# Kernel optimization log

Measured on AMD Instinct MI355X. Metric: run time of the kernel, lower is better.

The kernel has to match this reference:

```python
import jax, jax.numpy as jnp
import numpy as np
from jax import lax

UP = 2
K = 3
IN_C, OUT_C = 64, 64
PAD = K // 2  # 1
WEIGHT_GAIN = 1.0 / np.sqrt(IN_C * K * K)
ACT_GAIN = np.sqrt(2.0)  # lrelu def_gain
CLAMP = 256.0
LRELU_ALPHA = 0.2


def setup_inputs() -> dict:
    key = jax.random.key(0)
    k1, k2 = jax.random.split(key)
    x = jax.random.normal(k1, (16, IN_C, 128, 128), dtype=jnp.float32)
    weight = jax.random.normal(k2, (OUT_C, IN_C, K, K), dtype=jnp.float32)
    bias = jnp.zeros((OUT_C,), dtype=jnp.float32)
    # upfirdn2d.setup_filter((1,3,3,1)): outer product, normalized to sum 1
    a = jnp.array([1.0, 3.0, 3.0, 1.0], dtype=jnp.float32)
    f = jnp.outer(a, a)
    f = f / jnp.sum(f)  # 4x4 separable FIR filter
    return {"x": x, "weight": weight, "bias": bias, "f": f}


def _upfirdn2d_up2(x, f):
    # zero-insertion upsample by 2 + pad + FIR filter, gain = up**2
    N, C, H, W = x.shape
    fw = f.shape[-1]  # 4
    # conv2d_resample padding adjustment for up>1 on top of base padding k//2
    p0 = PAD + (fw + UP - 1) // 2  # 3
    p1 = PAD + (fw - UP) // 2      # 2
    fk = jnp.tile((f * (UP * UP))[None, None], (C, 1, 1, 1))  # [C,1,4,4] depthwise
    # lhs_dilation=2 gives 2H-1 samples; add (UP-1) extra right/bottom zeros to
    # match upfirdn's 2H zero-inserted signal.
    return lax.conv_general_dilated(
        x, fk, window_strides=(1, 1),
        padding=((p0, p1 + UP - 1), (p0, p1 + UP - 1)),
        lhs_dilation=(UP, UP),
        feature_group_count=C,
        dimension_numbers=("NCHW", "OIHW", "NCHW"))


def reference(x, weight, bias, f):
    h = _upfirdn2d_up2(x, f)  # [N, C, 2H+2, 2W+2]
    # conv: flip_weight = (up == 1) = False -> true convolution (flip kernel)
    w = (weight * WEIGHT_GAIN)[:, :, ::-1, ::-1]
    y = lax.conv_general_dilated(
        h, w, window_strides=(1, 1), padding="VALID",
        dimension_numbers=("NCHW", "OIHW", "NCHW"))  # [N, OUT_C, 2H, 2W]
    # fused bias + lrelu + gain + clamp (bias_act with gain=1)
    y = y + bias[None, :, None, None]
    y = jnp.where(y >= 0, y, LRELU_ALPHA * y) * ACT_GAIN
    y = jnp.clip(y, -CLAMP, CLAMP)
    return y
```

## Files before the change

### kernel.cpp

```cpp
#include <hip/hip_runtime.h>

typedef float f32x16 __attribute__((ext_vector_type(16)));
typedef float f32x4  __attribute__((ext_vector_type(4)));
typedef float f32x2  __attribute__((ext_vector_type(2)));
typedef short bf16x8 __attribute__((ext_vector_type(8)));

#define NB 16
#define CI 64
#define CO 64
#define Hh 128
#define Ww 128

__device__ short g_A[9 * 4 * 8 * 64 * 8];
__device__ short g_xh[(size_t)NB * Hh * Ww * CI];

__device__ inline short f2bf(float f) {
  union { float f; unsigned u; } v; v.f = f;
  unsigned r = (v.u + 0x7FFF + ((v.u >> 16) & 1)) >> 16;
  return (short)r;
}

__global__ __launch_bounds__(256) void prep(const float* __restrict__ x,
                                            const float* __restrict__ w) {
  const int tid = threadIdx.x;
  if (blockIdx.x >= 2048) {
    const int base = (blockIdx.x - 2048) * 2304;
    #pragma unroll
    for (int i = 0; i < 9; ++i) {
      const int ef = base + i * 256 + tid;
      const int e   = ef & 7;
      const int l   = (ef >> 3) & 63;
      const int mg  = (ef >> 9) & 7;
      const int ks  = (ef >> 12) & 3;
      const int tap = ef >> 14;
      const int r   = l & 31;
      const int px  = r & 1;
      const int py  = mg >> 2;
      const int oc  = (mg & 3) * 16 + (r >> 1);
      const int ic  = ks * 16 + (l >> 5) * 8 + e;
      const int dyi = tap / 3, dxi = tap % 3;
      const int my = 2 * dyi + 1 - py;
      const int mx = 2 * dxi + 1 - px;
      const float FF[4] = {0.25f, 0.75f, 0.75f, 0.25f};
      const float* wp = w + (oc * CI + ic) * 9;
      float s = 0.f;
      #pragma unroll
      for (int ky = 0; ky < 3; ++ky) {
        const int iy = my - ky;
        if (iy < 0 || iy > 3) continue;
        #pragma unroll
        for (int kx = 0; kx < 3; ++kx) {
          const int ix = mx - kx;
          if (ix < 0 || ix > 3) continue;
          s += wp[(2 - ky) * 3 + (2 - kx)] * (FF[iy] * FF[ix]);
        }
      }
      g_A[ef] = f2bf(s * (1.0f / 24.0f));
    }
    return;
  }
  __shared__ alignas(16) char xt[64 * 512];
  const int b = blockIdx.x;
  const int n = b >> 7, y = b & 127;
  #pragma unroll
  for (int it = 0; it < 8; ++it) {
    const int idx = tid + it * 256;
    const int ic = idx >> 5, xq = idx & 31;
    const f32x4 v = *(const f32x4*)(x + (((size_t)n * CI + ic) * Hh + y) * Ww + xq * 4);
    *(f32x4*)(xt + ic * 512 + ((xq * 16) ^ (((ic >> 3) & 7) * 16))) = v;
  }
  __syncthreads();
  #pragma unroll
  for (int it = 0; it < 4; ++it) {
    const int idx = tid + it * 256;
    const int icb = idx & 7, xp = idx >> 3;
    bf16x8 o;
    #pragma unroll
    for (int j = 0; j < 8; ++j) {
      const int ic = icb * 8 + j;
      const float f = *(const float*)(xt + ic * 512 + (((xp >> 2) * 16) ^ (icb * 16)) + (xp & 3) * 4);
      o[j] = f2bf(f);
    }
    *(bf16x8*)(g_xh + (((size_t)n * Hh + y) * Ww + xp) * CI + icb * 8) = o;
  }
}

#define CH_STR 1728

__global__ __launch_bounds__(256, 3) void mfma_conv(const float* __restrict__ bias,
                                                    float* __restrict__ out) {
  __shared__ alignas(16) char xs[8 * CH_STR];

  const int tid = threadIdx.x;
  const int l   = tid & 63;
  const int wid = tid >> 6;
  const int n   = blockIdx.y;
  const int ty0 = blockIdx.x >> 3, tx0 = blockIdx.x & 7;
  const int qb  = ty0 * 4, pb = tx0 * 16;

  bf16x8 a[4][2];
  #pragma unroll
  for (int ks = 0; ks < 4; ++ks)
    #pragma unroll
    for (int mf = 0; mf < 2; ++mf)
      a[ks][mf] = *(const bf16x8*)(g_A + (ks * 8 + wid * 2 + mf) * 512 + l * 8);

  const size_t xbase = (size_t)n * (Hh * Ww * CI);
  for (int u = tid; u < 864; u += 256) {
    const int icb8 = u & 7, pix = u >> 3;
    const int yy = pix / 18, xx = pix - yy * 18;
    const int gy = qb - 1 + yy, gx = pb - 1 + xx;
    bf16x8 v = {};
    if ((unsigned)gy < (unsigned)Hh && (unsigned)gx < (unsigned)Ww)
      v = *(const bf16x8*)(g_xh + xbase + (size_t)(gy * Ww + gx) * CI + icb8 * 8);
    *(bf16x8*)(xs + icb8 * CH_STR + pix * 16) = v;
  }
  __syncthreads();

  f32x16 acc[2][2];
  #pragma unroll
  for (int mf = 0; mf < 2; ++mf)
    #pragma unroll
    for (int nf = 0; nf < 2; ++nf)
      #pragma unroll
      for (int r = 0; r < 16; ++r) acc[mf][nf][r] = 0.f;

  const int col = l & 31, kg2 = l >> 5;
  const int p = col & 15, qh = col >> 4;
  int bbase[2];
  #pragma unroll
  for (int nf = 0; nf < 2; ++nf)
    bbase[nf] = kg2 * CH_STR + ((nf * 2 + qh) * 18 + p) * 16;

  #pragma unroll
  for (int tap = 0; tap < 9; ++tap) {
    const int dyi = tap / 3, dxi = tap % 3;
    const int bsh = (dyi * 18 + dxi) * 16;
    #pragma unroll
    for (int ks = 0; ks < 4; ++ks) {
      bf16x8 b[2];
      #pragma unroll
      for (int nf = 0; nf < 2; ++nf)
        b[nf] = *(const bf16x8*)(xs + bbase[nf] + ks * (2 * CH_STR) + bsh);
      __builtin_amdgcn_s_setprio(1);
      #pragma unroll
      for (int mf = 0; mf < 2; ++mf)
        #pragma unroll
        for (int nf = 0; nf < 2; ++nf)
          acc[mf][nf] = __builtin_amdgcn_mfma_f32_32x32x16_bf16(a[ks][mf], b[nf], acc[mf][nf], 0, 0, 0);
      __builtin_amdgcn_s_setprio(0);
      if (tap < 8) {
        #pragma unroll
        for (int mf = 0; mf < 2; ++mf)
          a[ks][mf] = *(const bf16x8*)(g_A + (((tap + 1) * 4 + ks) * 8 + wid * 2 + mf) * 512 + l * 8);
      }
    }
  }

  float* outp = out + ((size_t)(n * CO) << 16);
  #pragma unroll
  for (int mf = 0; mf < 2; ++mf) {
    const int mg = wid * 2 + mf;
    const int py = mg >> 2, och = mg & 3;
    #pragma unroll
    for (int nf = 0; nf < 2; ++nf) {
      const int q = nf * 2 + qh;
      const int y = 2 * (qb + q) + py;
      const int xd = 2 * (pb + p);
      #pragma unroll
      for (int rp = 0; rp < 8; ++rp) {
        const int oc = och * 16 + (rp & 1) + 4 * (rp >> 1) + 2 * kg2;
        const float bj = bias[oc];
        float v0 = acc[mf][nf][2 * rp]     + bj;
        float v1 = acc[mf][nf][2 * rp + 1] + bj;
        v0 = (v0 >= 0.f ? v0 : 0.2f * v0) * 1.4142135623730951f;
        v1 = (v1 >= 0.f ? v1 : 0.2f * v1) * 1.4142135623730951f;
        v0 = fminf(256.f, fmaxf(-256.f, v0));
        v1 = fminf(256.f, fmaxf(-256.f, v1));
        f32x2 o; o[0] = v0; o[1] = v1;
        __builtin_nontemporal_store(o, (f32x2*)(outp + ((size_t)oc << 16) + y * 256 + xd));
      }
    }
  }
}

extern "C" void kernel_launch(void* const* d_in, const int* in_sizes, int n_in,
                              void* d_out, int out_size, void* d_ws, size_t ws_size,
                              hipStream_t stream) {
  const float* x    = (const float*)d_in[0];
  const float* w    = (const float*)d_in[1];
  const float* bias = (const float*)d_in[2];
  float* out = (float*)d_out;

  prep<<<2112, 256, 0, stream>>>(x, w);
  mfma_conv<<<dim3(256, NB), 256, 0, stream>>>(bias, out);
}
```

Baseline: 121.6 us.

## Retile conv to full-width rows with LDS-staged weights split across blocks

Restructures the MFMA conv so each block covers four full-width input rows and a quarter of the output-phase/channel groups. The block now stages input channels in two halves in LDS and double-buffers the weight fragments into LDS via global_load_lds, instead of holding them in registers. The aim is a larger N-tile per wave (4 fragments) for more MFMA reuse per B load, plus fewer redundant halo loads. In exchange, the input tile is reloaded by four blocks, LDS use rises so occupancy drops to two blocks per CU, there is extra per-tap synchronisation, and output stores switch from nontemporal to normal stores.

```diff
diff --git a/kernel.cpp b/kernel.cpp
--- a/kernel.cpp
+++ b/kernel.cpp
@@ -11,7 +11,7 @@
 #define Hh 128
 #define Ww 128
 
-__device__ short g_A[9 * 4 * 8 * 64 * 8];
+__device__ short g_A[9 * 2 * 8 * 2 * 64 * 8];
 __device__ short g_xh[(size_t)NB * Hh * Ww * CI];
 
 __device__ inline short f2bf(float f) {
@@ -28,16 +28,17 @@
     #pragma unroll
     for (int i = 0; i < 9; ++i) {
       const int ef = base + i * 256 + tid;
-      const int e   = ef & 7;
-      const int l   = (ef >> 3) & 63;
-      const int mg  = (ef >> 9) & 7;
-      const int ks  = (ef >> 12) & 3;
-      const int tap = ef >> 14;
+      const int e     = ef & 7;
+      const int l     = (ef >> 3) & 63;
+      const int ks_in = (ef >> 9) & 1;
+      const int mg    = (ef >> 10) & 7;
+      const int kc    = (ef >> 13) & 1;
+      const int tap   = ef >> 14;
       const int r   = l & 31;
       const int px  = r & 1;
       const int py  = mg >> 2;
       const int oc  = (mg & 3) * 16 + (r >> 1);
-      const int ic  = ks * 16 + (l >> 5) * 8 + e;
+      const int ic  = (kc * 2 + ks_in) * 16 + (l >> 5) * 8 + e;
       const int dyi = tap / 3, dxi = tap % 3;
       const int my = 2 * dyi + 1 - py;
       const int mx = 2 * dxi + 1 - px;
@@ -85,88 +86,94 @@
   }
 }
 
-#define CH_STR 1728
-
-__global__ __launch_bounds__(256, 3) void mfma_conv(const float* __restrict__ bias,
+#define CH 12480
+#define AB 49920
+
+__global__ __launch_bounds__(256, 2) void mfma_conv(const float* __restrict__ bias,
                                                     float* __restrict__ out) {
-  __shared__ alignas(16) char xs[8 * CH_STR];
+  __shared__ alignas(16) char lds[58112];
 
   const int tid = threadIdx.x;
   const int l   = tid & 63;
   const int wid = tid >> 6;
   const int n   = blockIdx.y;
-  const int ty0 = blockIdx.x >> 3, tx0 = blockIdx.x & 7;
-  const int qb  = ty0 * 4, pb = tx0 * 16;
-
-  bf16x8 a[4][2];
-  #pragma unroll
-  for (int ks = 0; ks < 4; ++ks)
-    #pragma unroll
-    for (int mf = 0; mf < 2; ++mf)
-      a[ks][mf] = *(const bf16x8*)(g_A + (ks * 8 + wid * 2 + mf) * 512 + l * 8);
-
+  const int z   = blockIdx.x & 3;
+  const int qt  = blockIdx.x >> 2;
+  const int qb  = qt * 4;
+
+  auto stageA = [&](int tap, int kc, int buf) {
+    const char* gs = (const char*)g_A + ((tap * 2 + kc) * 16 + 4 * z) * 1024 + tid * 16;
+    char* ls = (char*)lds + AB + buf * 4096 + wid * 1024;
+    __builtin_amdgcn_global_load_lds(
+        (const __attribute__((address_space(1))) unsigned*)gs,
+        (__attribute__((address_space(3))) unsigned*)ls, 16, 0, 0);
+  };
+
+  stageA(0, 0, 0);
+
+  f32x16 acc[2][4];
+  #pragma unroll
+  for (int mf = 0; mf < 2; ++mf)
+    #pragma unroll
+    for (int nf = 0; nf < 4; ++nf)
+      #pragma unroll
+      for (int r = 0; r < 16; ++r) acc[mf][nf][r] = 0.f;
+
+  const int col = l & 31, kg2 = l >> 5;
   const size_t xbase = (size_t)n * (Hh * Ww * CI);
-  for (int u = tid; u < 864; u += 256) {
-    const int icb8 = u & 7, pix = u >> 3;
-    const int yy = pix / 18, xx = pix - yy * 18;
-    const int gy = qb - 1 + yy, gx = pb - 1 + xx;
-    bf16x8 v = {};
-    if ((unsigned)gy < (unsigned)Hh && (unsigned)gx < (unsigned)Ww)
-      v = *(const bf16x8*)(g_xh + xbase + (size_t)(gy * Ww + gx) * CI + icb8 * 8);
-    *(bf16x8*)(xs + icb8 * CH_STR + pix * 16) = v;
-  }
-  __syncthreads();
-
-  f32x16 acc[2][2];
-  #pragma unroll
-  for (int mf = 0; mf < 2; ++mf)
-    #pragma unroll
-    for (int nf = 0; nf < 2; ++nf)
-      #pragma unroll
-      for (int r = 0; r < 16; ++r) acc[mf][nf][r] = 0.f;
-
-  const int col = l & 31, kg2 = l >> 5;
-  const int p = col & 15, qh = col >> 4;
-  int bbase[2];
-  #pragma unroll
-  for (int nf = 0; nf < 2; ++nf)
-    bbase[nf] = kg2 * CH_STR + ((nf * 2 + qh) * 18 + p) * 16;
-
-  #pragma unroll
-  for (int tap = 0; tap < 9; ++tap) {
-    const int dyi = tap / 3, dxi = tap % 3;
-    const int bsh = (dyi * 18 + dxi) * 16;
-    #pragma unroll
-    for (int ks = 0; ks < 4; ++ks) {
-      bf16x8 b[2];
-      #pragma unroll
-      for (int nf = 0; nf < 2; ++nf)
-        b[nf] = *(const bf16x8*)(xs + bbase[nf] + ks * (2 * CH_STR) + bsh);
-      __builtin_amdgcn_s_setprio(1);
-      #pragma unroll
-      for (int mf = 0; mf < 2; ++mf)
-        #pragma unroll
-        for (int nf = 0; nf < 2; ++nf)
-          acc[mf][nf] = __builtin_amdgcn_mfma_f32_32x32x16_bf16(a[ks][mf], b[nf], acc[mf][nf], 0, 0, 0);
-      __builtin_amdgcn_s_setprio(0);
-      if (tap < 8) {
+
+  #pragma unroll
+  for (int kc = 0; kc < 2; ++kc) {
+    __syncthreads();
+    for (int u = tid; u < 3120; u += 256) {
+      const int icb = u & 3, idx = u >> 2;
+      const int row = idx / 130, colh = idx - row * 130;
+      const int gy = qb - 1 + row, gx = colh - 1;
+      bf16x8 v = {};
+      if ((unsigned)gy < (unsigned)Hh && (unsigned)gx < (unsigned)Ww)
+        v = *(const bf16x8*)(g_xh + xbase + (size_t)(gy * Ww + gx) * CI + kc * 32 + icb * 8);
+      *(bf16x8*)(lds + icb * CH + idx * 16) = v;
+    }
+    #pragma unroll
+    for (int tap = 0; tap < 9; ++tap) {
+      const int s = kc * 9 + tap;
+      asm volatile("s_waitcnt vmcnt(0)" ::: "memory");
+      __syncthreads();
+      if (tap < 8) stageA(tap + 1, kc, (s + 1) & 1);
+      else if (kc == 0) stageA(0, 1, (s + 1) & 1);
+      const int dyi = tap / 3, dxi = tap % 3;
+      const int abuf = AB + (s & 1) * 4096;
+      #pragma unroll
+      for (int ks = 0; ks < 2; ++ks) {
+        bf16x8 a[2], b[4];
         #pragma unroll
         for (int mf = 0; mf < 2; ++mf)
-          a[ks][mf] = *(const bf16x8*)(g_A + (((tap + 1) * 4 + ks) * 8 + wid * 2 + mf) * 512 + l * 8);
+          a[mf] = *(const bf16x8*)(lds + abuf + (mf * 2 + ks) * 1024 + l * 16);
+        #pragma unroll
+        for (int nf = 0; nf < 4; ++nf)
+          b[nf] = *(const bf16x8*)(lds + (ks * 2 + kg2) * CH +
+                                   ((wid + dyi) * 130 + nf * 32 + col + dxi) * 16);
+        __builtin_amdgcn_s_setprio(1);
+        #pragma unroll
+        for (int mf = 0; mf < 2; ++mf)
+          #pragma unroll
+          for (int nf = 0; nf < 4; ++nf)
+            acc[mf][nf] = __builtin_amdgcn_mfma_f32_32x32x16_bf16(a[mf], b[nf], acc[mf][nf], 0, 0, 0);
+        __builtin_amdgcn_s_setprio(0);
       }
     }
   }
 
   float* outp = out + ((size_t)(n * CO) << 16);
+  const int q = qb + wid;
   #pragma unroll
   for (int mf = 0; mf < 2; ++mf) {
-    const int mg = wid * 2 + mf;
+    const int mg = 2 * z + mf;
     const int py = mg >> 2, och = mg & 3;
-    #pragma unroll
-    for (int nf = 0; nf < 2; ++nf) {
-      const int q = nf * 2 + qh;
-      const int y = 2 * (qb + q) + py;
-      const int xd = 2 * (pb + p);
+    const int y = 2 * q + py;
+    #pragma unroll
+    for (int nf = 0; nf < 4; ++nf) {
+      const int xd = 2 * (nf * 32 + col);
       #pragma unroll
       for (int rp = 0; rp < 8; ++rp) {
         const int oc = och * 16 + (rp & 1) + 4 * (rp >> 1) + 2 * kg2;
@@ -178,7 +185,7 @@
         v0 = fminf(256.f, fmaxf(-256.f, v0));
         v1 = fminf(256.f, fmaxf(-256.f, v1));
         f32x2 o; o[0] = v0; o[1] = v1;
-        __builtin_nontemporal_store(o, (f32x2*)(outp + ((size_t)oc << 16) + y * 256 + xd));
+        *(f32x2*)(outp + ((size_t)oc << 16) + y * 256 + xd) = o;
       }
     }
   }
@@ -193,5 +200,5 @@
   float* out = (float*)d_out;
 
   prep<<<2112, 256, 0, stream>>>(x, w);
-  mfma_conv<<<dim3(256, NB), 256, 0, stream>>>(bias, out);
-}
+  mfma_conv<<<dim3(128, NB), 256, 0, stream>>>(bias, out);
+}
```

Measured after the change: 161.9 us. 33.1% more time.

## Double spatial tile height per block and split warps over M and N

Applied to the files above, without the earlier changes.

Each block now covers 8 input rows instead of 4, with warps arranged 2x2 over output-channel groups and pixel rows. Each warp loops over two M halves, reloading weight fragments for each, so the halo overhead of the staged input tile is amortised over more pixels. The grid is halved, which reduces parallelism to 2048 blocks, and LDS per block grows. Output stores also switch from nontemporal to regular stores.

```diff
diff --git a/kernel.cpp b/kernel.cpp
--- a/kernel.cpp
+++ b/kernel.cpp
@@ -85,7 +85,7 @@
   }
 }
 
-#define CH_STR 1728
+#define CH_STR 2896
 
 __global__ __launch_bounds__(256, 3) void mfma_conv(const float* __restrict__ bias,
                                                     float* __restrict__ out) {
@@ -94,19 +94,14 @@
   const int tid = threadIdx.x;
   const int l   = tid & 63;
   const int wid = tid >> 6;
+  const int wm  = wid >> 1;
+  const int wn  = wid & 1;
   const int n   = blockIdx.y;
   const int ty0 = blockIdx.x >> 3, tx0 = blockIdx.x & 7;
-  const int qb  = ty0 * 4, pb = tx0 * 16;
-
-  bf16x8 a[4][2];
-  #pragma unroll
-  for (int ks = 0; ks < 4; ++ks)
-    #pragma unroll
-    for (int mf = 0; mf < 2; ++mf)
-      a[ks][mf] = *(const bf16x8*)(g_A + (ks * 8 + wid * 2 + mf) * 512 + l * 8);
+  const int qb  = ty0 * 8, pb = tx0 * 16;
 
   const size_t xbase = (size_t)n * (Hh * Ww * CI);
-  for (int u = tid; u < 864; u += 256) {
+  for (int u = tid; u < 1440; u += 256) {
     const int icb8 = u & 7, pix = u >> 3;
     const int yy = pix / 18, xx = pix - yy * 18;
     const int gy = qb - 1 + yy, gx = pb - 1 + xx;
@@ -117,68 +112,79 @@
   }
   __syncthreads();
 
-  f32x16 acc[2][2];
-  #pragma unroll
-  for (int mf = 0; mf < 2; ++mf)
-    #pragma unroll
-    for (int nf = 0; nf < 2; ++nf)
-      #pragma unroll
-      for (int r = 0; r < 16; ++r) acc[mf][nf][r] = 0.f;
-
   const int col = l & 31, kg2 = l >> 5;
   const int p = col & 15, qh = col >> 4;
   int bbase[2];
   #pragma unroll
   for (int nf = 0; nf < 2; ++nf)
-    bbase[nf] = kg2 * CH_STR + ((nf * 2 + qh) * 18 + p) * 16;
-
-  #pragma unroll
-  for (int tap = 0; tap < 9; ++tap) {
-    const int dyi = tap / 3, dxi = tap % 3;
-    const int bsh = (dyi * 18 + dxi) * 16;
-    #pragma unroll
-    for (int ks = 0; ks < 4; ++ks) {
-      bf16x8 b[2];
+    bbase[nf] = kg2 * CH_STR + ((wn * 4 + nf * 2 + qh) * 18 + p) * 16;
+
+  float* outp = out + ((size_t)(n * CO) << 16);
+
+  #pragma unroll
+  for (int h = 0; h < 2; ++h) {
+    bf16x8 a[4][2];
+    #pragma unroll
+    for (int ks = 0; ks < 4; ++ks)
+      #pragma unroll
+      for (int m2 = 0; m2 < 2; ++m2)
+        a[ks][m2] = *(const bf16x8*)(g_A + (ks * 8 + wm * 4 + h * 2 + m2) * 512 + l * 8);
+
+    f32x16 acc[2][2];
+    #pragma unroll
+    for (int m2 = 0; m2 < 2; ++m2)
       #pragma unroll
       for (int nf = 0; nf < 2; ++nf)
-        b[nf] = *(const bf16x8*)(xs + bbase[nf] + ks * (2 * CH_STR) + bsh);
-      __builtin_amdgcn_s_setprio(1);
-      #pragma unroll
-      for (int mf = 0; mf < 2; ++mf)
+        #pragma unroll
+        for (int r = 0; r < 16; ++r) acc[m2][nf][r] = 0.f;
+
+    #pragma unroll
+    for (int tap = 0; tap < 9; ++tap) {
+      const int dyi = tap / 3, dxi = tap % 3;
+      const int bsh = (dyi * 18 + dxi) * 16;
+      #pragma unroll
+      for (int ks = 0; ks < 4; ++ks) {
+        bf16x8 b[2];
         #pragma unroll
         for (int nf = 0; nf < 2; ++nf)
-          acc[mf][nf] = __builtin_amdgcn_mfma_f32_32x32x16_bf16(a[ks][mf], b[nf], acc[mf][nf], 0, 0, 0);
-      __builtin_amdgcn_s_setprio(0);
-      if (tap < 8) {
-        #pragma unroll
-        for (int mf = 0; mf < 2; ++mf)
-          a[ks][mf] = *(const bf16x8*)(g_A + (((tap + 1) * 4 + ks) * 8 + wid * 2 + mf) * 512 + l * 8);
+          b[nf] = *(const bf16x8*)(xs + bbase[nf] + ks * (2 * CH_STR) + bsh);
+        __builtin_amdgcn_s_setprio(1);
+        #pragma unroll
+        for (int m2 = 0; m2 < 2; ++m2)
+          #pragma unroll
+          for (int nf = 0; nf < 2; ++nf)
+            acc[m2][nf] = __builtin_amdgcn_mfma_f32_32x32x16_bf16(a[ks][m2], b[nf], acc[m2][nf], 0, 0, 0);
+        __builtin_amdgcn_s_setprio(0);
+        if (tap < 8) {
+          #pragma unroll
+          for (int m2 = 0; m2 < 2; ++m2)
+            a[ks][m2] = *(const bf16x8*)(g_A + (((tap + 1) * 4 + ks) * 8 + wm * 4 + h * 2 + m2) * 512 + l * 8);
+        }
       }
     }
-  }
-
-  float* outp = out + ((size_t)(n * CO) << 16);
-  #pragma unroll
-  for (int mf = 0; mf < 2; ++mf) {
-    const int mg = wid * 2 + mf;
-    const int py = mg >> 2, och = mg & 3;
-    #pragma unroll
-    for (int nf = 0; nf < 2; ++nf) {
-      const int q = nf * 2 + qh;
-      const int y = 2 * (qb + q) + py;
-      const int xd = 2 * (pb + p);
-      #pragma unroll
-      for (int rp = 0; rp < 8; ++rp) {
-        const int oc = och * 16 + (rp & 1) + 4 * (rp >> 1) + 2 * kg2;
-        const float bj = bias[oc];
-        float v0 = acc[mf][nf][2 * rp]     + bj;
-        float v1 = acc[mf][nf][2 * rp + 1] + bj;
-        v0 = (v0 >= 0.f ? v0 : 0.2f * v0) * 1.4142135623730951f;
-        v1 = (v1 >= 0.f ? v1 : 0.2f * v1) * 1.4142135623730951f;
-        v0 = fminf(256.f, fmaxf(-256.f, v0));
-        v1 = fminf(256.f, fmaxf(-256.f, v1));
-        f32x2 o; o[0] = v0; o[1] = v1;
-        __builtin_nontemporal_store(o, (f32x2*)(outp + ((size_t)oc << 16) + y * 256 + xd));
+
+    #pragma unroll
+    for (int m2 = 0; m2 < 2; ++m2) {
+      const int mg = wm * 4 + h * 2 + m2;
+      const int py = mg >> 2, och = mg & 3;
+      #pragma unroll
+      for (int nf = 0; nf < 2; ++nf) {
+        const int q = wn * 4 + nf * 2 + qh;
+        const int y = 2 * (qb + q) + py;
+        const int xd = 2 * (pb + p);
+        #pragma unroll
+        for (int rp = 0; rp < 8; ++rp) {
+          const int oc = och * 16 + (rp & 1) + 4 * (rp >> 1) + 2 * kg2;
+          const float bj = bias[oc];
+          float v0 = acc[m2][nf][2 * rp]     + bj;
+          float v1 = acc[m2][nf][2 * rp + 1] + bj;
+          v0 = (v0 >= 0.f ? v0 : 0.2f * v0) * 1.4142135623730951f;
+          v1 = (v1 >= 0.f ? v1 : 0.2f * v1) * 1.4142135623730951f;
+          v0 = fminf(256.f, fmaxf(-256.f, v0));
+          v1 = fminf(256.f, fmaxf(-256.f, v1));
+          f32x2 o; o[0] = v0; o[1] = v1;
+          *(f32x2*)(outp + ((size_t)oc << 16) + y * 256 + xd) = o;
+        }
       }
     }
   }
@@ -193,5 +199,5 @@
   float* out = (float*)d_out;
 
   prep<<<2112, 256, 0, stream>>>(x, w);
-  mfma_conv<<<dim3(256, NB), 256, 0, stream>>>(bias, out);
-}
+  mfma_conv<<<dim3(128, NB), 256, 0, stream>>>(bias, out);
+}
```

Measured after the change: 147.6 us. +21.3%, slower.
